# Kernel optimization log

Measured on AMD Instinct MI355X. Metric: run time of the kernel, lower is better.

The kernel has to match this reference:

```python
import jax, jax.numpy as jnp
import numpy as np

B, S, N = 16, 128, 64            # batch, sentence length, padded KB-word slots per sentence
E, DK, H, L = 128, 128, 128, 32  # char embed, kb embed, per-direction hidden (hidden_size=2H), labels
CHAR_NUM, KB_NUM = 8000, 200000


def setup_inputs():
    key = jax.random.key(0)
    ks = jax.random.split(key, 40)
    u = lambda k, sh: jax.random.uniform(k, sh, jnp.float32, -0.08, 0.08)
    inp = {
        "char_ids": jax.random.randint(ks[0], (B, S), 0, CHAR_NUM),
        "kb_word_ids": jax.random.randint(ks[1], (B, N), 0, KB_NUM),
        "word_begin": jax.random.randint(ks[2], (B, N), 0, S),
        "word_len": jax.random.randint(ks[3], (B, N), 0, 6),
        "label": jax.random.randint(ks[4], (B, S), 0, L),
        "sequence_length": jax.random.randint(ks[5], (B,), S // 2, S + 1),
        "char_emb": u(ks[6], (CHAR_NUM, E)),
        "kb_emb": u(ks[7], (KB_NUM, DK)),
        "dense_W": u(ks[8], (2 * H, L)),
        "dense_b": jnp.zeros((L,), jnp.float32),
        "crf_T": u(ks[9], (L, L)),
    }
    i = 10
    for p in ("f", "r"):
        inp[p + "_Wcx"] = u(ks[i], (E, 4 * H))
        inp[p + "_Wch"] = u(ks[i + 1], (H, 4 * H))
        inp[p + "_bc"] = jnp.zeros((4 * H,), jnp.float32)
        inp[p + "_Wwx"] = u(ks[i + 2], (DK, 3 * H))
        inp[p + "_Wwh"] = u(ks[i + 3], (H, 3 * H))
        inp[p + "_bw"] = jnp.zeros((3 * H,), jnp.float32)
        inp[p + "_Wlx"] = u(ks[i + 4], (E, H))
        inp[p + "_Wlc"] = u(ks[i + 5], (H, H))
        inp[p + "_bl"] = jnp.zeros((H,), jnp.float32)
        i += 6
    return inp


def _lattice_dir(X, Xw, begin, end, pos_valid, word_valid,
                 Wcx, Wch, bc, Wwx, Wwh, bw, Wlx, Wlc, bl):
    # X:[S,E] chars in scan order, Xw:[N,DK] KB words, begin/end:[N] span indices
    # in scan order (end inclusive), pos_valid:[S] bool, word_valid:[N] bool.
    Xg = X @ Wcx + bc    # [S,4H] hoisted char-gate input projection
    Xl = X @ Wlx + bl    # [S,H]  hoisted link-gate input projection
    Wg = Xw @ Wwx + bw   # [N,3H] hoisted word-gate input projection

    def step(carry, t):
        h_hist, c_hist = carry                 # [S+1,H]; slot k = state after step k-1
        h_prev, c_prev = h_hist[t], c_hist[t]
        gi, gf, go, gg = jnp.split(Xg[t] + h_prev @ Wch, 4)
        i = jax.nn.sigmoid(gi); f = jax.nn.sigmoid(gf)
        o = jax.nn.sigmoid(go); g = jnp.tanh(gg)
        # word cells: built from the state just before each word's begin position
        hb, cb = h_hist[begin], c_hist[begin]  # [N,H]
        wi, wf, wg = jnp.split(Wg + hb @ Wwh, 3, axis=1)
        cw = jax.nn.sigmoid(wf) * cb + jax.nn.sigmoid(wi) * jnp.tanh(wg)  # [N,H]
        lg = jax.nn.sigmoid(Xl[t] + cw @ Wlc)  # [N,H] link gates
        wmask = ((end == t) & word_valid).astype(X.dtype)[:, None]
        ew = jnp.exp(lg) * wmask
        ec = jnp.exp(i)
        c_lat = (ec * g + (ew * cw).sum(0)) / (ec + ew.sum(0))  # gate-normalized merge
        c_std = f * c_prev + i * g             # plain LSTM step when no word ends at t
        c_t = jnp.where(wmask.sum() > 0, c_lat, c_std)
        h_t = o * jnp.tanh(c_t)
        v = pos_valid[t]
        h_hist = h_hist.at[t + 1].set(jnp.where(v, h_t, h_prev))
        c_hist = c_hist.at[t + 1].set(jnp.where(v, c_t, c_prev))
        return (h_hist, c_hist), jnp.where(v, h_t, jnp.zeros_like(h_t))

    init = (jnp.zeros((S + 1, H), X.dtype), jnp.zeros((S + 1, H), X.dtype))
    _, hs = jax.lax.scan(step, init, jnp.arange(S))
    return hs  # [S,H]


def _forward(char_ids, kb_word_ids, word_begin, word_len, label, sequence_length,
             char_emb, kb_emb, dense_W, dense_b, crf_T, fparams, rparams):
    X = char_emb[char_ids]            # [B,S,E]
    Xw = kb_emb[kb_word_ids]          # [B,N,DK]
    end = jnp.minimum(word_begin + word_len, S - 1)   # inclusive span end
    word_valid = end < sequence_length[:, None]       # whole span inside sentence
    pos = jnp.arange(S)
    pv_f = pos[None, :] < sequence_length[:, None]
    fwd = jax.vmap(lambda x, xw, b, e, pv, wv:
                   _lattice_dir(x, xw, b, e, pv, wv, *fparams))(
        X, Xw, word_begin, end, pv_f, word_valid)
    # backward direction: flip time axis; span (b,e) maps to (S-1-e, S-1-b)
    pv_r = pos[None, :] >= (S - sequence_length)[:, None]
    bwd = jax.vmap(lambda x, xw, b, e, pv, wv:
                   _lattice_dir(x, xw, b, e, pv, wv, *rparams))(
        X[:, ::-1], Xw, S - 1 - end, S - 1 - word_begin, pv_r, word_valid)[:, ::-1]
    feats = jnp.concatenate([fwd, bwd], axis=-1)      # [B,S,2H]
    logits = feats @ dense_W + dense_b                # [B,S,L]
    # CRF negative log-likelihood
    mask = pv_f.astype(logits.dtype)                  # [B,S]
    emit = jnp.take_along_axis(logits, label[..., None], axis=2)[..., 0]
    trans = crf_T[label[:, :-1], label[:, 1:]]
    gold = (emit * mask).sum(1) + (trans * mask[:, 1:]).sum(1)

    def fstep(alpha, xs):
        logit_t, m_t = xs
        new = jax.scipy.special.logsumexp(alpha[:, :, None] + crf_T[None], axis=1) + logit_t
        return jnp.where(m_t[:, None] > 0, new, alpha), None

    alpha, _ = jax.lax.scan(fstep, logits[:, 0],
                            (logits[:, 1:].transpose(1, 0, 2), mask[:, 1:].T))
    logZ = jax.scipy.special.logsumexp(alpha, axis=1)
    return jnp.mean(logZ - gold)


def reference(char_ids, kb_word_ids, word_begin, word_len, label, sequence_length,
              char_emb, kb_emb, dense_W, dense_b, crf_T,
              f_Wcx, f_Wch, f_bc, f_Wwx, f_Wwh, f_bw, f_Wlx, f_Wlc, f_bl,
              r_Wcx, r_Wch, r_bc, r_Wwx, r_Wwh, r_bw, r_Wlx, r_Wlc, r_bl):
    fparams = (f_Wcx, f_Wch, f_bc, f_Wwx, f_Wwh, f_bw, f_Wlx, f_Wlc, f_bl)
    rparams = (r_Wcx, r_Wch, r_bc, r_Wwx, r_Wwh, r_bw, r_Wlx, r_Wlc, r_bl)
    return _forward(char_ids, kb_word_ids, word_begin, word_len, label, sequence_length,
                    char_emb, kb_emb, dense_W, dense_b, crf_T, fparams, rparams)
```

## Files before the change

kernel.cpp:

```cpp
#include <hip/hip_runtime.h>


typedef _Float16 f16x2 __attribute__((ext_vector_type(2)));

__device__ __forceinline__ float sigm(float x) { return 1.f / (1.f + __expf(-x)); }
__device__ __forceinline__ float tanh_fast(float x) {
    return 1.f - 2.f / (__expf(2.f * x) + 1.f);
}
__device__ __forceinline__ void bar_lgkm() {
    asm volatile("s_waitcnt lgkmcnt(0)\n\ts_barrier" ::: "memory");
}

#if defined(__has_builtin)
#if __has_builtin(__builtin_amdgcn_fdot2)
#define FDOT2(a, b, c) __builtin_amdgcn_fdot2((a), (b), (c), false)
#endif
#endif
#ifndef FDOT2
__device__ __forceinline__ float fdot2_sw(f16x2 a, f16x2 b, float c) {
    return fmaf((float)a.x, (float)b.x, fmaf((float)a.y, (float)b.y, c));
}
#define FDOT2(a, b, c) fdot2_sw((a), (b), (c))
#endif

template <int K, int J, int RPB, int BLK>
__global__ __launch_bounds__(BLK)
void gemm_pair(const float* __restrict__ emb, const int* __restrict__ idx,
               const float* __restrict__ W0, const float* __restrict__ W1,
               const float* __restrict__ b0, const float* __restrict__ b1,
               float* __restrict__ out, int rowsTotal, int Sdim, int revmode)
{
    constexpr int NJ4 = J / 4;
    constexpr int RT  = BLK / NJ4;
    constexpr int RPT = RPB / RT;
    static_assert(BLK % NJ4 == 0 && RPB % RT == 0, "layout");
    const int y = blockIdx.y;
    const float* __restrict__ W    = y ? W1 : W0;
    const float* __restrict__ bias = y ? b1 : b0;
    float* __restrict__ outp = out + (size_t)y * rowsTotal * J;
    const int rev = (revmode && y) ? 1 : 0;

    __shared__ __align__(16) float xs[RPB * K];
    __shared__ const float* srcs[RPB];
    const int tid = threadIdx.x;
    const int r0 = blockIdx.x * RPB;
    if (tid < RPB) {
        const int row = r0 + tid;
        const float* s = nullptr;
        if (row < rowsTotal) {
            if (idx) {
                const int bb = row / Sdim, tt = row - bb * Sdim;
                const int ts = rev ? (Sdim - 1 - tt) : tt;
                s = emb + (size_t)idx[bb * Sdim + ts] * K;
            } else {
                s = emb + (size_t)row * K;
            }
        }
        srcs[tid] = s;
    }
    __syncthreads();
    constexpr int NQ = RPB * K / 4;
    for (int q = tid; q < NQ; q += BLK) {
        const int rr = q / (K / 4), qq = q - rr * (K / 4);
        const float4* s = (const float4*)srcs[rr];
        ((float4*)xs)[q] = s ? s[qq] : make_float4(0.f, 0.f, 0.f, 0.f);
    }
    __syncthreads();

    const int jq = tid % NJ4;
    const int rg = tid / NJ4;
    float4 acc[RPT];
#pragma unroll
    for (int r = 0; r < RPT; ++r) acc[r] = make_float4(0.f, 0.f, 0.f, 0.f);
    const float4* __restrict__ W4 = (const float4*)W;
#pragma unroll 4
    for (int k = 0; k < K; ++k) {
        const float4 wv = W4[(size_t)k * NJ4 + jq];
#pragma unroll
        for (int r = 0; r < RPT; ++r) {
            const float xv = xs[(rg * RPT + r) * K + k];
            acc[r].x = fmaf(xv, wv.x, acc[r].x);
            acc[r].y = fmaf(xv, wv.y, acc[r].y);
            acc[r].z = fmaf(xv, wv.z, acc[r].z);
            acc[r].w = fmaf(xv, wv.w, acc[r].w);
        }
    }
    const float4 bv = ((const float4*)bias)[jq];
#pragma unroll
    for (int r = 0; r < RPT; ++r) {
        const int row = r0 + rg * RPT + r;
        if (row < rowsTotal)
            ((float4*)outp)[(size_t)row * NJ4 + jq] =
                make_float4(acc[r].x + bv.x, acc[r].y + bv.y,
                            acc[r].z + bv.z, acc[r].w + bv.w);
    }
}

#define HH_BYTES (129 * 128 * 2)
#define CH_BYTES (129 * 128 * 4)
#define LAT_DYN_SMEM (HH_BYTES + CH_BYTES)

__global__ __launch_bounds__(512, 2)
void lattice_kernel(const float* __restrict__ Xg,
                    const float* __restrict__ Xl,
                    const float* __restrict__ Wgp,
                    const float* __restrict__ Wch_f, const float* __restrict__ Wch_r,
                    const float* __restrict__ Wwh_f, const float* __restrict__ Wwh_r,
                    const float* __restrict__ Wlc_f, const float* __restrict__ Wlc_r,
                    const int* __restrict__ word_begin, const int* __restrict__ word_len,
                    const int* __restrict__ seqlen,
                    float* __restrict__ feats)
{
    extern __shared__ __align__(16) char dyn_smem[];
    _Float16* hh = (_Float16*)dyn_smem;
    float*    ch = (float*)(dyn_smem + HH_BYTES);

    const int bdid = blockIdx.x;
    const int b = bdid >> 1, dir = bdid & 1;
    const int tid = threadIdx.x;
    const int kc = tid >> 7;
    const int jj = tid & 127;

    const float* Wch = dir ? Wch_r : Wch_f;
    const float* Wwh = dir ? Wwh_r : Wwh_f;
    const float* Wlc = dir ? Wlc_r : Wlc_f;

    f16x2 wch2[64];
    {
        const float* base = Wch + (size_t)(kc * 32) * 512 + jj;
#pragma unroll
        for (int g = 0; g < 4; ++g)
#pragma unroll
            for (int u2 = 0; u2 < 16; ++u2) {
                f16x2 v;
                v.x = (_Float16)base[(size_t)(2 * u2) * 512 + g * 128];
                v.y = (_Float16)base[(size_t)(2 * u2 + 1) * 512 + g * 128];
                wch2[g * 16 + u2] = v;
            }
    }
    f16x2 wwh2[48];
    {
        const float* base = Wwh + (size_t)(kc * 32) * 384 + jj;
#pragma unroll
        for (int g = 0; g < 3; ++g)
#pragma unroll
            for (int u2 = 0; u2 < 16; ++u2) {
                f16x2 v;
                v.x = (_Float16)base[(size_t)(2 * u2) * 384 + g * 128];
                v.y = (_Float16)base[(size_t)(2 * u2 + 1) * 384 + g * 128];
                wwh2[g * 16 + u2] = v;
            }
    }
    f16x2 wlc2[16];
    {
        const float* base = Wlc + (size_t)(kc * 32) * 128 + jj;
#pragma unroll
        for (int u2 = 0; u2 < 16; ++u2) {
            f16x2 v;
            v.x = (_Float16)base[(size_t)(2 * u2) * 128];
            v.y = (_Float16)base[(size_t)(2 * u2 + 1) * 128];
            wlc2[u2] = v;
        }
    }

    __shared__ __align__(16) float part[2048];
    __shared__ __align__(16) float wpart[2 * 1536];
    __shared__ __align__(16) float lpart[2 * 512];
    __shared__ __align__(16) _Float16 cw2s[2 * 128];
    __shared__ int ev_start[129];
    __shared__ int cnts[128];
    __shared__ int fills[128];
    __shared__ short ev_word[64];
    __shared__ short wbeg_s[64];

    const int sl = seqlen[b];

    if (tid < 128) { cnts[tid] = 0; fills[tid] = 0; }
    __syncthreads();
    int myvalid = 0, myed = 0;
    if (tid < 64) {
        const int bg = word_begin[b * 64 + tid];
        const int ln = word_len[b * 64 + tid];
        int ef = bg + ln; if (ef > 127) ef = 127;
        myvalid = (ef < sl);
        const int bd_ = dir ? (127 - ef) : bg;
        const int ed_ = dir ? (127 - bg) : ef;
        wbeg_s[tid] = (short)bd_;
        myed = ed_;
        if (myvalid) atomicAdd(&cnts[ed_], 1);
    }
    __syncthreads();
    if (tid == 0) {
        int run = 0; ev_start[0] = 0;
        for (int t = 0; t < 128; ++t) { run += cnts[t]; ev_start[t + 1] = run; }
    }
    __syncthreads();
    if (tid < 64 && myvalid) {
        const int pos = atomicAdd(&fills[myed], 1);
        ev_word[ev_start[myed] + pos] = (short)tid;
    }
    if (tid < 128) { hh[tid] = (_Float16)0.f; ch[tid] = 0.f; }
    __syncthreads();

    const float* Xg_b = Xg + ((size_t)dir * 2048 + (size_t)b * 128) * 512;
    const float* Xl_b = Xl + ((size_t)dir * 2048 + (size_t)b * 128) * 128;
    const float* Wg_b = Wgp + ((size_t)dir * 1024 + (size_t)b * 64) * 384;

    float h_reg = 0.f, c_reg = 0.f;
    float xg_cur = Xg_b[tid];

    for (int t = 0; t < 128; ++t) {
        const int e0 = ev_start[t];
        const int E  = ev_start[t + 1] - e0;
        const int ec0 = E < 2 ? E : 2;

        int bgs[2] = {0, 0};
        float wgp[2][3];
        float xl = 0.f;
#pragma unroll
        for (int s = 0; s < 2; ++s)
            if (s < ec0) {
                const int w = ev_word[e0 + s];
                bgs[s] = wbeg_s[w];
                if (tid < 128) {
                    const float* wgr = Wg_b + (size_t)w * 384;
                    wgp[s][0] = wgr[tid]; wgp[s][1] = wgr[128 + tid]; wgp[s][2] = wgr[256 + tid];
                }
            }
        if (E > 0 && tid < 128) xl = Xl_b[(size_t)t * 128 + tid];
        const float xg_nxt = (t < 127) ? Xg_b[(size_t)(t + 1) * 512 + tid] : 0.f;

        {
            const f16x2* hrow = (const f16x2*)(hh + (size_t)t * 128) + kc * 16;
            f16x2 hv[16];
#pragma unroll
            for (int u2 = 0; u2 < 16; ++u2) hv[u2] = hrow[u2];
            float p0 = 0.f, p1 = 0.f, p2 = 0.f, p3 = 0.f;
#pragma unroll
            for (int u2 = 0; u2 < 16; ++u2) {
                p0 = FDOT2(wch2[u2],      hv[u2], p0);
                p1 = FDOT2(wch2[16 + u2], hv[u2], p1);
                p2 = FDOT2(wch2[32 + u2], hv[u2], p2);
                p3 = FDOT2(wch2[48 + u2], hv[u2], p3);
            }
            if      (kc == 0) p0 += xg_cur;
            else if (kc == 1) p1 += xg_cur;
            else if (kc == 2) p2 += xg_cur;
            else              p3 += xg_cur;
            part[kc * 512 +       jj] = p0;
            part[kc * 512 + 128 + jj] = p1;
            part[kc * 512 + 256 + jj] = p2;
            part[kc * 512 + 384 + jj] = p3;
        }
#pragma unroll
        for (int s = 0; s < 2; ++s)
            if (s < ec0) {
                const f16x2* hbrow = (const f16x2*)(hh + (size_t)bgs[s] * 128) + kc * 16;
                float q0 = 0.f, q1 = 0.f, q2 = 0.f;
#pragma unroll
                for (int u2 = 0; u2 < 16; ++u2) {
                    const f16x2 hb = hbrow[u2];
                    q0 = FDOT2(wwh2[u2],      hb, q0);
                    q1 = FDOT2(wwh2[16 + u2], hb, q1);
                    q2 = FDOT2(wwh2[32 + u2], hb, q2);
                }
                wpart[s * 1536 + kc * 384 +       jj] = q0;
                wpart[s * 1536 + kc * 384 + 128 + jj] = q1;
                wpart[s * 1536 + kc * 384 + 256 + jj] = q2;
            }
        bar_lgkm();

        float gi = 0.f, gf = 0.f, go = 0.f, gg = 0.f;
        float cwreg[2] = {0.f, 0.f};
        if (tid < 128) {
            const float a0 = part[tid]       + part[512 + tid]  + part[1024 + tid] + part[1536 + tid];
            const float a1 = part[128 + tid] + part[640 + tid]  + part[1152 + tid] + part[1664 + tid];
            const float a2 = part[256 + tid] + part[768 + tid]  + part[1280 + tid] + part[1792 + tid];
            const float a3 = part[384 + tid] + part[896 + tid]  + part[1408 + tid] + part[1920 + tid];
            gi = sigm(a0); gf = sigm(a1); go = sigm(a2); gg = tanh_fast(a3);
#pragma unroll
            for (int s = 0; s < 2; ++s)
                if (s < ec0) {
                    const int sb = s * 1536;
                    const float cb = ch[(size_t)bgs[s] * 128 + tid];
                    const float wi = wgp[s][0] + wpart[sb + tid]       + wpart[sb + 384 + tid] + wpart[sb + 768 + tid]  + wpart[sb + 1152 + tid];
                    const float wf = wgp[s][1] + wpart[sb + 128 + tid] + wpart[sb + 512 + tid] + wpart[sb + 896 + tid]  + wpart[sb + 1280 + tid];
                    const float wv = wgp[s][2] + wpart[sb + 256 + tid] + wpart[sb + 640 + tid] + wpart[sb + 1024 + tid] + wpart[sb + 1408 + tid];
                    const float cwv = sigm(wf) * cb + sigm(wi) * tanh_fast(wv);
                    cwreg[s] = cwv;
                    cw2s[s * 128 + tid] = (_Float16)cwv;
                }
        }

        float accn = 0.f, accd = 0.f;
        if (E > 0) {
            bar_lgkm();
            const int nc = (E + 1) >> 1;
            for (int c = 0; c < nc; ++c) {
                const int base = c * 2;
                const int en = (E - base) < 2 ? (E - base) : 2;
#pragma unroll
                for (int s = 0; s < 2; ++s)
                    if (s < en) {
                        const f16x2* cwrow = (const f16x2*)(cw2s + s * 128) + kc * 16;
                        float r = 0.f;
#pragma unroll
                        for (int u2 = 0; u2 < 16; ++u2) r = FDOT2(wlc2[u2], cwrow[u2], r);
                        lpart[s * 512 + kc * 128 + jj] = r;
                    }
                const int nb = base + 2;
                int nn = E - nb; nn = nn < 0 ? 0 : (nn > 2 ? 2 : nn);
                int bgs2[2] = {0, 0};
                float wgp2[2][3];
#pragma unroll
                for (int s = 0; s < 2; ++s)
                    if (s < nn) {
                        const int w = ev_word[e0 + nb + s];
                        bgs2[s] = wbeg_s[w];
                        if (tid < 128) {
                            const float* wgr = Wg_b + (size_t)w * 384;
                            wgp2[s][0] = wgr[tid]; wgp2[s][1] = wgr[128 + tid]; wgp2[s][2] = wgr[256 + tid];
                        }
                    }
#pragma unroll
                for (int s = 0; s < 2; ++s)
                    if (s < nn) {
                        const f16x2* hbrow = (const f16x2*)(hh + (size_t)bgs2[s] * 128) + kc * 16;
                        float q0 = 0.f, q1 = 0.f, q2 = 0.f;
#pragma unroll
                        for (int u2 = 0; u2 < 16; ++u2) {
                            const f16x2 hb = hbrow[u2];
                            q0 = FDOT2(wwh2[u2],      hb, q0);
                            q1 = FDOT2(wwh2[16 + u2], hb, q1);
                            q2 = FDOT2(wwh2[32 + u2], hb, q2);
                        }
                        wpart[s * 1536 + kc * 384 +       jj] = q0;
                        wpart[s * 1536 + kc * 384 + 128 + jj] = q1;
                        wpart[s * 1536 + kc * 384 + 256 + jj] = q2;
                    }
                bar_lgkm();
                if (tid < 128) {
#pragma unroll
                    for (int s = 0; s < 2; ++s)
                        if (s < en) {
                            const float lg = sigm(xl + lpart[s * 512 + tid] + lpart[s * 512 + 128 + tid]
                                                     + lpart[s * 512 + 256 + tid] + lpart[s * 512 + 384 + tid]);
                            const float ew = __expf(lg);
                            accn = fmaf(ew, cwreg[s], accn);
                            accd += ew;
                        }
#pragma unroll
                    for (int s = 0; s < 2; ++s)
                        if (s < nn) {
                            const int sb = s * 1536;
                            const float cb = ch[(size_t)bgs2[s] * 128 + tid];
                            const float wi = wgp2[s][0] + wpart[sb + tid]       + wpart[sb + 384 + tid] + wpart[sb + 768 + tid]  + wpart[sb + 1152 + tid];
                            const float wf = wgp2[s][1] + wpart[sb + 128 + tid] + wpart[sb + 512 + tid] + wpart[sb + 896 + tid]  + wpart[sb + 1280 + tid];
                            const float wv = wgp2[s][2] + wpart[sb + 256 + tid] + wpart[sb + 640 + tid] + wpart[sb + 1024 + tid] + wpart[sb + 1408 + tid];
                            const float cwv = sigm(wf) * cb + sigm(wi) * tanh_fast(wv);
                            cwreg[s] = cwv;
                            cw2s[s * 128 + tid] = (_Float16)cwv;
                        }
                }
                if (c + 1 < nc) bar_lgkm();
            }
        }

        if (tid < 128) {
            float c_t;
            if (E > 0) {
                const float ec = __expf(gi);
                c_t = (ec * gg + accn) / (ec + accd);
            } else {
                c_t = gf * c_reg + gi * gg;
            }
            const float h_t = go * tanh_fast(c_t);
            const bool v = dir ? (t >= 128 - sl) : (t < sl);
            const float hn = v ? h_t : h_reg;
            const float cn = v ? c_t : c_reg;
            h_reg = hn; c_reg = cn;
            hh[(size_t)(t + 1) * 128 + tid] = (_Float16)hn;
            ch[(size_t)(t + 1) * 128 + tid] = cn;
        }
        xg_cur = xg_nxt;
        bar_lgkm();
    }

    for (int i = tid; i < 128 * 128; i += 512) {
        const int t = i >> 7, j = i & 127;
        const bool v = dir ? (t >= 128 - sl) : (t < sl);
        const float hv = v ? (float)hh[(size_t)(t + 1) * 128 + j] : 0.f;
        const int s = dir ? (127 - t) : t;
        feats[((size_t)b * 128 + s) * 256 + dir * 128 + j] = hv;
    }
}

__global__ void crf_kernel(const float* __restrict__ logits,
                           const int* __restrict__ label,
                           const int* __restrict__ seqlen,
                           const float* __restrict__ T,
                           float* __restrict__ out_part)
{
    const int half = threadIdx.x >> 5;
    const int j    = threadIdx.x & 31;
    const int b    = blockIdx.x * 2 + half;

    float Tc[32];
#pragma unroll
    for (int i = 0; i < 32; ++i) Tc[i] = T[i * 32 + j];

    const float* lg = logits + (size_t)b * 128 * 32;
    const int* lab = label + b * 128;
    const int sl = seqlen[b];

    float g = 0.f;
#pragma unroll
    for (int r = 0; r < 4; ++r) {
        const int t = j + r * 32;
        if (t < sl) {
            g += lg[t * 32 + lab[t]];
            if (t >= 1) g += T[lab[t - 1] * 32 + lab[t]];
        }
    }
#pragma unroll
    for (int m = 16; m; m >>= 1) g += __shfl_xor(g, m, 32);

    __shared__ __align__(16) float alpha_s[2][32];
    float av = lg[j];
    alpha_s[half][j] = av;
    __syncthreads();
    for (int t = 1; t < 128; ++t) {
        float a[32];
        const float4* ap = (const float4*)alpha_s[half];
#pragma unroll
        for (int q = 0; q < 8; ++q) {
            const float4 v = ap[q];
            a[4 * q] = v.x; a[4 * q + 1] = v.y; a[4 * q + 2] = v.z; a[4 * q + 3] = v.w;
        }
        float m = -1e30f;
#pragma unroll
        for (int i = 0; i < 32; ++i) m = fmaxf(m, a[i] + Tc[i]);
        float s = 0.f;
#pragma unroll
        for (int i = 0; i < 32; ++i) s += __expf(a[i] + Tc[i] - m);
        float nv = m + __logf(s) + lg[t * 32 + j];
        if (t >= sl) nv = av;
        av = nv;
        __syncthreads();
        alpha_s[half][j] = av;
        __syncthreads();
    }
    float m2 = av;
#pragma unroll
    for (int m = 16; m; m >>= 1) m2 = fmaxf(m2, __shfl_xor(m2, m, 32));
    float s2 = __expf(av - m2);
#pragma unroll
    for (int m = 16; m; m >>= 1) s2 += __shfl_xor(s2, m, 32);
    if (j == 0) out_part[b] = (m2 + __logf(s2)) - g;
}

__global__ void finalize_kernel(const float* __restrict__ partb, float* __restrict__ out)
{
    if (threadIdx.x == 0 && blockIdx.x == 0) {
        float s = 0.f;
        for (int i = 0; i < 16; i++) s += partb[i];
        out[0] = s * (1.f / 16.f);
    }
}

extern "C" void kernel_launch(void* const* d_in, const int* in_sizes, int n_in,
                              void* d_out, int out_size, void* d_ws, size_t ws_size,
                              hipStream_t stream)
{
    (void)in_sizes; (void)n_in; (void)out_size; (void)ws_size;
    const int*   char_ids    = (const int*)d_in[0];
    const int*   kb_word_ids = (const int*)d_in[1];
    const int*   word_begin  = (const int*)d_in[2];
    const int*   word_len    = (const int*)d_in[3];
    const int*   label       = (const int*)d_in[4];
    const int*   seqlen      = (const int*)d_in[5];
    const float* char_emb    = (const float*)d_in[6];
    const float* kb_emb      = (const float*)d_in[7];
    const float* dense_W     = (const float*)d_in[8];
    const float* dense_b     = (const float*)d_in[9];
    const float* crf_T       = (const float*)d_in[10];
    const float* f_Wcx = (const float*)d_in[11];
    const float* f_Wch = (const float*)d_in[12];
    const float* f_bc  = (const float*)d_in[13];
    const float* f_Wwx = (const float*)d_in[14];
    const float* f_Wwh = (const float*)d_in[15];
    const float* f_bw  = (const float*)d_in[16];
    const float* f_Wlx = (const float*)d_in[17];
    const float* f_Wlc = (const float*)d_in[18];
    const float* f_bl  = (const float*)d_in[19];
    const float* r_Wcx = (const float*)d_in[20];
    const float* r_Wch = (const float*)d_in[21];
    const float* r_bc  = (const float*)d_in[22];
    const float* r_Wwx = (const float*)d_in[23];
    const float* r_Wwh = (const float*)d_in[24];
    const float* r_bw  = (const float*)d_in[25];
    const float* r_Wlx = (const float*)d_in[26];
    const float* r_Wlc = (const float*)d_in[27];
    const float* r_bl  = (const float*)d_in[28];

    float* ws = (float*)d_ws;
    size_t o = 0;
    float* Xg     = ws + o; o += (size_t)2 * 2048 * 512;
    float* Xl     = ws + o; o += (size_t)2 * 2048 * 128;
    float* Wg     = ws + o; o += (size_t)2 * 1024 * 384;
    float* feats  = ws + o; o += (size_t)2048 * 256;
    float* logits = ws + o; o += (size_t)2048 * 32;
    float* partb  = ws + o; o += 16;

    gemm_pair<128, 512, 8, 256><<<dim3(256, 2), 256, 0, stream>>>(
        char_emb, char_ids, f_Wcx, r_Wcx, f_bc, r_bc, Xg, 2048, 128, 1);
    gemm_pair<128, 128, 8, 256><<<dim3(256, 2), 256, 0, stream>>>(
        char_emb, char_ids, f_Wlx, r_Wlx, f_bl, r_bl, Xl, 2048, 128, 1);
    gemm_pair<128, 384, 8, 192><<<dim3(128, 2), 192, 0, stream>>>(
        kb_emb, kb_word_ids, f_Wwx, r_Wwx, f_bw, r_bw, Wg, 1024, 64, 0);

    lattice_kernel<<<32, 512, LAT_DYN_SMEM, stream>>>(
        Xg, Xl, Wg, f_Wch, r_Wch, f_Wwh, r_Wwh, f_Wlc, r_Wlc,
        word_begin, word_len, seqlen, feats);

    gemm_pair<256, 32, 16, 128><<<dim3(128, 1), 128, 0, stream>>>(
        feats, nullptr, dense_W, dense_W, dense_b, dense_b, logits, 2048, 128, 0);
    crf_kernel<<<8, 64, 0, stream>>>(logits, label, seqlen, crf_T, partb);
    finalize_kernel<<<1, 64, 0, stream>>>(partb, (float*)d_out);
}
```

Baseline: 540.6 us.

## Store hoisted projections in fp16 and stage them in LDS for the lattice scan

The input-projection GEMMs now write fp16 outputs, with Xg/Xl in a time-interleaved layout of 8-step blocks. The lattice kernel stages the per-sentence word projections in shared memory and double-buffers 8-step chunks of Xg/Xl in LDS, which takes global loads off the sequential critical path. The cell-state history is reduced to an 8-slot ring in LDS. The CRF kernel preloads logits and labels into shared memory, and the GEMM unroll and rows-per-block are raised. Risks are fp16 precision loss on the projections, and the c ring buffer breaks if a word span is longer than 8 steps (lengths here are at most 6).

```diff
diff --git a/kernel.cpp b/kernel.cpp
--- a/kernel.cpp
+++ b/kernel.cpp
@@ -23,12 +23,12 @@
 #define FDOT2(a, b, c) fdot2_sw((a), (b), (c))
 #endif
 
-template <int K, int J, int RPB, int BLK>
+template <int K, int J, int RPB, int BLK, int OMODE>
 __global__ __launch_bounds__(BLK)
 void gemm_pair(const float* __restrict__ emb, const int* __restrict__ idx,
                const float* __restrict__ W0, const float* __restrict__ W1,
                const float* __restrict__ b0, const float* __restrict__ b1,
-               float* __restrict__ out, int rowsTotal, int Sdim, int revmode)
+               void* __restrict__ out, int rowsTotal, int Sdim, int revmode)
 {
     constexpr int NJ4 = J / 4;
     constexpr int RT  = BLK / NJ4;
@@ -37,7 +37,6 @@
     const int y = blockIdx.y;
     const float* __restrict__ W    = y ? W1 : W0;
     const float* __restrict__ bias = y ? b1 : b0;
-    float* __restrict__ outp = out + (size_t)y * rowsTotal * J;
     const int rev = (revmode && y) ? 1 : 0;
 
     __shared__ __align__(16) float xs[RPB * K];
@@ -73,7 +72,7 @@
 #pragma unroll
     for (int r = 0; r < RPT; ++r) acc[r] = make_float4(0.f, 0.f, 0.f, 0.f);
     const float4* __restrict__ W4 = (const float4*)W;
-#pragma unroll 4
+#pragma unroll 8
     for (int k = 0; k < K; ++k) {
         const float4 wv = W4[(size_t)k * NJ4 + jq];
 #pragma unroll
@@ -89,21 +88,30 @@
 #pragma unroll
     for (int r = 0; r < RPT; ++r) {
         const int row = r0 + rg * RPT + r;
-        if (row < rowsTotal)
-            ((float4*)outp)[(size_t)row * NJ4 + jq] =
-                make_float4(acc[r].x + bv.x, acc[r].y + bv.y,
-                            acc[r].z + bv.z, acc[r].w + bv.w);
-    }
-}
-
-#define HH_BYTES (129 * 128 * 2)
-#define CH_BYTES (129 * 128 * 4)
-#define LAT_DYN_SMEM (HH_BYTES + CH_BYTES)
-
-__global__ __launch_bounds__(512, 2)
-void lattice_kernel(const float* __restrict__ Xg,
-                    const float* __restrict__ Xl,
-                    const float* __restrict__ Wgp,
+        if (row >= rowsTotal) continue;
+        float v4[4] = {acc[r].x + bv.x, acc[r].y + bv.y, acc[r].z + bv.z, acc[r].w + bv.w};
+        if constexpr (OMODE == 0) {
+            float* o32 = (float*)out + (size_t)y * rowsTotal * J;
+            ((float4*)o32)[(size_t)row * NJ4 + jq] = make_float4(v4[0], v4[1], v4[2], v4[3]);
+        } else if constexpr (OMODE == 1) {
+            _Float16* o16 = (_Float16*)out + (size_t)y * rowsTotal * J;
+            const size_t base = ((size_t)(row >> 3)) * (size_t)(J * 8) + (row & 7);
+#pragma unroll
+            for (int c = 0; c < 4; ++c)
+                o16[base + (size_t)(jq * 4 + c) * 8] = (_Float16)v4[c];
+        } else {
+            _Float16* o16 = (_Float16*)out + (size_t)y * rowsTotal * J;
+#pragma unroll
+            for (int c = 0; c < 4; ++c)
+                o16[(size_t)row * J + jq * 4 + c] = (_Float16)v4[c];
+        }
+    }
+}
+
+__global__ __launch_bounds__(512, 1)
+void lattice_kernel(const _Float16* __restrict__ Xg16,
+                    const _Float16* __restrict__ Xl16,
+                    const _Float16* __restrict__ Wg16G,
                     const float* __restrict__ Wch_f, const float* __restrict__ Wch_r,
                     const float* __restrict__ Wwh_f, const float* __restrict__ Wwh_r,
                     const float* __restrict__ Wlc_f, const float* __restrict__ Wlc_r,
@@ -111,10 +119,6 @@
                     const int* __restrict__ seqlen,
                     float* __restrict__ feats)
 {
-    extern __shared__ __align__(16) char dyn_smem[];
-    _Float16* hh = (_Float16*)dyn_smem;
-    float*    ch = (float*)(dyn_smem + HH_BYTES);
-
     const int bdid = blockIdx.x;
     const int b = bdid >> 1, dir = bdid & 1;
     const int tid = threadIdx.x;
@@ -125,6 +129,21 @@
     const float* Wwh = dir ? Wwh_r : Wwh_f;
     const float* Wlc = dir ? Wlc_r : Wlc_f;
 
+    __shared__ __align__(16) _Float16 wg16[64 * 384];
+    __shared__ __align__(16) _Float16 hh[129 * 128];
+    __shared__ __align__(16) float    c_win[8 * 128];
+    __shared__ __align__(16) float part[2048];
+    __shared__ __align__(16) float wpart[2 * 1536];
+    __shared__ __align__(16) float lpart[2 * 512];
+    __shared__ __align__(16) _Float16 cw2s[2 * 128];
+    __shared__ __align__(16) _Float16 xgbuf[2 * 4096];
+    __shared__ __align__(16) _Float16 xlbuf[2 * 1024];
+    __shared__ int ev_start[129];
+    __shared__ int cnts[128];
+    __shared__ int fills[128];
+    __shared__ short ev_word[64];
+    __shared__ short wbeg_s[64];
+
     f16x2 wch2[64];
     {
         const float* base = Wch + (size_t)(kc * 32) * 512 + jj;
@@ -162,16 +181,6 @@
             wlc2[u2] = v;
         }
     }
-
-    __shared__ __align__(16) float part[2048];
-    __shared__ __align__(16) float wpart[2 * 1536];
-    __shared__ __align__(16) float lpart[2 * 512];
-    __shared__ __align__(16) _Float16 cw2s[2 * 128];
-    __shared__ int ev_start[129];
-    __shared__ int cnts[128];
-    __shared__ int fills[128];
-    __shared__ short ev_word[64];
-    __shared__ short wbeg_s[64];
 
     const int sl = seqlen[b];
 
@@ -199,191 +208,205 @@
         const int pos = atomicAdd(&fills[myed], 1);
         ev_word[ev_start[myed] + pos] = (short)tid;
     }
-    if (tid < 128) { hh[tid] = (_Float16)0.f; ch[tid] = 0.f; }
-    __syncthreads();
-
-    const float* Xg_b = Xg + ((size_t)dir * 2048 + (size_t)b * 128) * 512;
-    const float* Xl_b = Xl + ((size_t)dir * 2048 + (size_t)b * 128) * 128;
-    const float* Wg_b = Wgp + ((size_t)dir * 1024 + (size_t)b * 64) * 384;
+    if (tid < 128) { hh[tid] = (_Float16)0.f; c_win[tid] = 0.f; }
+
+    {
+        const uint4* WgV = (const uint4*)(Wg16G + ((size_t)dir * 1024 + (size_t)b * 64) * 384);
+        uint4 wtmp[6];
+#pragma unroll
+        for (int i = 0; i < 6; ++i) wtmp[i] = WgV[i * 512 + tid];
+#pragma unroll
+        for (int i = 0; i < 6; ++i) ((uint4*)wg16)[i * 512 + tid] = wtmp[i];
+    }
+
+    const uint4* XgV = (const uint4*)(Xg16 + ((size_t)dir * 2048 + (size_t)b * 128) * 512);
+    const uint4* XlV = (const uint4*)(Xl16 + ((size_t)dir * 2048 + (size_t)b * 128) * 128);
+    uint4 xg_pre = XgV[tid];
+    uint4 xl_pre = make_uint4(0, 0, 0, 0);
+    if (tid < 128) xl_pre = XlV[tid];
+    __syncthreads();
 
     float h_reg = 0.f, c_reg = 0.f;
-    float xg_cur = Xg_b[tid];
-
-    for (int t = 0; t < 128; ++t) {
-        const int e0 = ev_start[t];
-        const int E  = ev_start[t + 1] - e0;
-        const int ec0 = E < 2 ? E : 2;
-
-        int bgs[2] = {0, 0};
-        float wgp[2][3];
-        float xl = 0.f;
-#pragma unroll
-        for (int s = 0; s < 2; ++s)
-            if (s < ec0) {
-                const int w = ev_word[e0 + s];
-                bgs[s] = wbeg_s[w];
-                if (tid < 128) {
-                    const float* wgr = Wg_b + (size_t)w * 384;
-                    wgp[s][0] = wgr[tid]; wgp[s][1] = wgr[128 + tid]; wgp[s][2] = wgr[256 + tid];
-                }
-            }
-        if (E > 0 && tid < 128) xl = Xl_b[(size_t)t * 128 + tid];
-        const float xg_nxt = (t < 127) ? Xg_b[(size_t)(t + 1) * 512 + tid] : 0.f;
-
-        {
-            const f16x2* hrow = (const f16x2*)(hh + (size_t)t * 128) + kc * 16;
-            f16x2 hv[16];
-#pragma unroll
-            for (int u2 = 0; u2 < 16; ++u2) hv[u2] = hrow[u2];
-            float p0 = 0.f, p1 = 0.f, p2 = 0.f, p3 = 0.f;
-#pragma unroll
-            for (int u2 = 0; u2 < 16; ++u2) {
-                p0 = FDOT2(wch2[u2],      hv[u2], p0);
-                p1 = FDOT2(wch2[16 + u2], hv[u2], p1);
-                p2 = FDOT2(wch2[32 + u2], hv[u2], p2);
-                p3 = FDOT2(wch2[48 + u2], hv[u2], p3);
-            }
-            if      (kc == 0) p0 += xg_cur;
-            else if (kc == 1) p1 += xg_cur;
-            else if (kc == 2) p2 += xg_cur;
-            else              p3 += xg_cur;
-            part[kc * 512 +       jj] = p0;
-            part[kc * 512 + 128 + jj] = p1;
-            part[kc * 512 + 256 + jj] = p2;
-            part[kc * 512 + 384 + jj] = p3;
-        }
-#pragma unroll
-        for (int s = 0; s < 2; ++s)
-            if (s < ec0) {
-                const f16x2* hbrow = (const f16x2*)(hh + (size_t)bgs[s] * 128) + kc * 16;
-                float q0 = 0.f, q1 = 0.f, q2 = 0.f;
-#pragma unroll
-                for (int u2 = 0; u2 < 16; ++u2) {
-                    const f16x2 hb = hbrow[u2];
-                    q0 = FDOT2(wwh2[u2],      hb, q0);
-                    q1 = FDOT2(wwh2[16 + u2], hb, q1);
-                    q2 = FDOT2(wwh2[32 + u2], hb, q2);
-                }
-                wpart[s * 1536 + kc * 384 +       jj] = q0;
-                wpart[s * 1536 + kc * 384 + 128 + jj] = q1;
-                wpart[s * 1536 + kc * 384 + 256 + jj] = q2;
-            }
+
+    for (int tc = 0; tc < 16; ++tc) {
+        _Float16* xgc = xgbuf + (tc & 1) * 4096;
+        _Float16* xlc = xlbuf + (tc & 1) * 1024;
+        ((uint4*)xgc)[tid] = xg_pre;
+        if (tid < 128) ((uint4*)xlc)[tid] = xl_pre;
+        if (tc < 15) {
+            xg_pre = XgV[(tc + 1) * 512 + tid];
+            if (tid < 128) xl_pre = XlV[(tc + 1) * 128 + tid];
+        }
         bar_lgkm();
 
-        float gi = 0.f, gf = 0.f, go = 0.f, gg = 0.f;
-        float cwreg[2] = {0.f, 0.f};
-        if (tid < 128) {
-            const float a0 = part[tid]       + part[512 + tid]  + part[1024 + tid] + part[1536 + tid];
-            const float a1 = part[128 + tid] + part[640 + tid]  + part[1152 + tid] + part[1664 + tid];
-            const float a2 = part[256 + tid] + part[768 + tid]  + part[1280 + tid] + part[1792 + tid];
-            const float a3 = part[384 + tid] + part[896 + tid]  + part[1408 + tid] + part[1920 + tid];
-            gi = sigm(a0); gf = sigm(a1); go = sigm(a2); gg = tanh_fast(a3);
+        for (int u = 0; u < 8; ++u) {
+            const int t = tc * 8 + u;
+            const int e0 = ev_start[t];
+            const int E  = ev_start[t + 1] - e0;
+            const int ec0 = E < 2 ? E : 2;
+
+            int bgs[2] = {0, 0}, wid[2] = {0, 0};
 #pragma unroll
             for (int s = 0; s < 2; ++s)
                 if (s < ec0) {
-                    const int sb = s * 1536;
-                    const float cb = ch[(size_t)bgs[s] * 128 + tid];
-                    const float wi = wgp[s][0] + wpart[sb + tid]       + wpart[sb + 384 + tid] + wpart[sb + 768 + tid]  + wpart[sb + 1152 + tid];
-                    const float wf = wgp[s][1] + wpart[sb + 128 + tid] + wpart[sb + 512 + tid] + wpart[sb + 896 + tid]  + wpart[sb + 1280 + tid];
-                    const float wv = wgp[s][2] + wpart[sb + 256 + tid] + wpart[sb + 640 + tid] + wpart[sb + 1024 + tid] + wpart[sb + 1408 + tid];
-                    const float cwv = sigm(wf) * cb + sigm(wi) * tanh_fast(wv);
-                    cwreg[s] = cwv;
-                    cw2s[s * 128 + tid] = (_Float16)cwv;
+                    const int w = ev_word[e0 + s];
+                    wid[s] = w; bgs[s] = wbeg_s[w];
                 }
-        }
-
-        float accn = 0.f, accd = 0.f;
-        if (E > 0) {
+            const float xg = (float)xgc[tid * 8 + u];
+
+            {
+                const f16x2* hrow = (const f16x2*)(hh + (size_t)t * 128) + kc * 16;
+                f16x2 hv[16];
+#pragma unroll
+                for (int u2 = 0; u2 < 16; ++u2) hv[u2] = hrow[u2];
+                float p0 = 0.f, p1 = 0.f, p2 = 0.f, p3 = 0.f;
+#pragma unroll
+                for (int u2 = 0; u2 < 16; ++u2) {
+                    p0 = FDOT2(wch2[u2],      hv[u2], p0);
+                    p1 = FDOT2(wch2[16 + u2], hv[u2], p1);
+                    p2 = FDOT2(wch2[32 + u2], hv[u2], p2);
+                    p3 = FDOT2(wch2[48 + u2], hv[u2], p3);
+                }
+                if      (kc == 0) p0 += xg;
+                else if (kc == 1) p1 += xg;
+                else if (kc == 2) p2 += xg;
+                else              p3 += xg;
+                part[kc * 512 +       jj] = p0;
+                part[kc * 512 + 128 + jj] = p1;
+                part[kc * 512 + 256 + jj] = p2;
+                part[kc * 512 + 384 + jj] = p3;
+            }
+#pragma unroll
+            for (int s = 0; s < 2; ++s)
+                if (s < ec0) {
+                    const f16x2* hbrow = (const f16x2*)(hh + (size_t)bgs[s] * 128) + kc * 16;
+                    float q0 = 0.f, q1 = 0.f, q2 = 0.f;
+#pragma unroll
+                    for (int u2 = 0; u2 < 16; ++u2) {
+                        const f16x2 hb = hbrow[u2];
+                        q0 = FDOT2(wwh2[u2],      hb, q0);
+                        q1 = FDOT2(wwh2[16 + u2], hb, q1);
+                        q2 = FDOT2(wwh2[32 + u2], hb, q2);
+                    }
+                    wpart[s * 1536 + kc * 384 +       jj] = q0;
+                    wpart[s * 1536 + kc * 384 + 128 + jj] = q1;
+                    wpart[s * 1536 + kc * 384 + 256 + jj] = q2;
+                }
             bar_lgkm();
-            const int nc = (E + 1) >> 1;
-            for (int c = 0; c < nc; ++c) {
-                const int base = c * 2;
-                const int en = (E - base) < 2 ? (E - base) : 2;
+
+            float gi = 0.f, gf = 0.f, go = 0.f, gg = 0.f;
+            float cwreg[2] = {0.f, 0.f};
+            if (tid < 128) {
+                const float a0 = part[tid]       + part[512 + tid]  + part[1024 + tid] + part[1536 + tid];
+                const float a1 = part[128 + tid] + part[640 + tid]  + part[1152 + tid] + part[1664 + tid];
+                const float a2 = part[256 + tid] + part[768 + tid]  + part[1280 + tid] + part[1792 + tid];
+                const float a3 = part[384 + tid] + part[896 + tid]  + part[1408 + tid] + part[1920 + tid];
+                gi = sigm(a0); gf = sigm(a1); go = sigm(a2); gg = tanh_fast(a3);
 #pragma unroll
                 for (int s = 0; s < 2; ++s)
-                    if (s < en) {
-                        const f16x2* cwrow = (const f16x2*)(cw2s + s * 128) + kc * 16;
-                        float r = 0.f;
-#pragma unroll
-                        for (int u2 = 0; u2 < 16; ++u2) r = FDOT2(wlc2[u2], cwrow[u2], r);
-                        lpart[s * 512 + kc * 128 + jj] = r;
+                    if (s < ec0) {
+                        const int sb = s * 1536;
+                        const _Float16* wgr = wg16 + wid[s] * 384;
+                        const float wi = (float)wgr[tid]       + wpart[sb + tid]       + wpart[sb + 384 + tid] + wpart[sb + 768 + tid]  + wpart[sb + 1152 + tid];
+                        const float wf = (float)wgr[128 + tid] + wpart[sb + 128 + tid] + wpart[sb + 512 + tid] + wpart[sb + 896 + tid]  + wpart[sb + 1280 + tid];
+                        const float wv = (float)wgr[256 + tid] + wpart[sb + 256 + tid] + wpart[sb + 640 + tid] + wpart[sb + 1024 + tid] + wpart[sb + 1408 + tid];
+                        const float cb = c_win[(bgs[s] & 7) * 128 + tid];
+                        const float cwv = sigm(wf) * cb + sigm(wi) * tanh_fast(wv);
+                        cwreg[s] = cwv;
+                        cw2s[s * 128 + tid] = (_Float16)cwv;
                     }
-                const int nb = base + 2;
-                int nn = E - nb; nn = nn < 0 ? 0 : (nn > 2 ? 2 : nn);
-                int bgs2[2] = {0, 0};
-                float wgp2[2][3];
-#pragma unroll
-                for (int s = 0; s < 2; ++s)
-                    if (s < nn) {
-                        const int w = ev_word[e0 + nb + s];
-                        bgs2[s] = wbeg_s[w];
-                        if (tid < 128) {
-                            const float* wgr = Wg_b + (size_t)w * 384;
-                            wgp2[s][0] = wgr[tid]; wgp2[s][1] = wgr[128 + tid]; wgp2[s][2] = wgr[256 + tid];
-                        }
-                    }
-#pragma unroll
-                for (int s = 0; s < 2; ++s)
-                    if (s < nn) {
-                        const f16x2* hbrow = (const f16x2*)(hh + (size_t)bgs2[s] * 128) + kc * 16;
-                        float q0 = 0.f, q1 = 0.f, q2 = 0.f;
-#pragma unroll
-                        for (int u2 = 0; u2 < 16; ++u2) {
-                            const f16x2 hb = hbrow[u2];
-                            q0 = FDOT2(wwh2[u2],      hb, q0);
-                            q1 = FDOT2(wwh2[16 + u2], hb, q1);
-                            q2 = FDOT2(wwh2[32 + u2], hb, q2);
-                        }
-                        wpart[s * 1536 + kc * 384 +       jj] = q0;
-                        wpart[s * 1536 + kc * 384 + 128 + jj] = q1;
-                        wpart[s * 1536 + kc * 384 + 256 + jj] = q2;
-                    }
+            }
+
+            float accn = 0.f, accd = 0.f;
+            if (E > 0) {
                 bar_lgkm();
-                if (tid < 128) {
+                const int nc = (E + 1) >> 1;
+                for (int c = 0; c < nc; ++c) {
+                    const int base = c * 2;
+                    const int en = (E - base) < 2 ? (E - base) : 2;
 #pragma unroll
                     for (int s = 0; s < 2; ++s)
                         if (s < en) {
-                            const float lg = sigm(xl + lpart[s * 512 + tid] + lpart[s * 512 + 128 + tid]
-                                                     + lpart[s * 512 + 256 + tid] + lpart[s * 512 + 384 + tid]);
-                            const float ew = __expf(lg);
-                            accn = fmaf(ew, cwreg[s], accn);
-                            accd += ew;
+                            const f16x2* cwrow = (const f16x2*)(cw2s + s * 128) + kc * 16;
+                            float r = 0.f;
+#pragma unroll
+                            for (int u2 = 0; u2 < 16; ++u2) r = FDOT2(wlc2[u2], cwrow[u2], r);
+                            lpart[s * 512 + kc * 128 + jj] = r;
                         }
+                    const int nb = base + 2;
+                    int nn = E - nb; nn = nn < 0 ? 0 : (nn > 2 ? 2 : nn);
+                    int bgs2[2] = {0, 0}, wid2[2] = {0, 0};
 #pragma unroll
                     for (int s = 0; s < 2; ++s)
                         if (s < nn) {
-                            const int sb = s * 1536;
-                            const float cb = ch[(size_t)bgs2[s] * 128 + tid];
-                            const float wi = wgp2[s][0] + wpart[sb + tid]       + wpart[sb + 384 + tid] + wpart[sb + 768 + tid]  + wpart[sb + 1152 + tid];
-                            const float wf = wgp2[s][1] + wpart[sb + 128 + tid] + wpart[sb + 512 + tid] + wpart[sb + 896 + tid]  + wpart[sb + 1280 + tid];
-                            const float wv = wgp2[s][2] + wpart[sb + 256 + tid] + wpart[sb + 640 + tid] + wpart[sb + 1024 + tid] + wpart[sb + 1408 + tid];
-                            const float cwv = sigm(wf) * cb + sigm(wi) * tanh_fast(wv);
-                            cwreg[s] = cwv;
-                            cw2s[s * 128 + tid] = (_Float16)cwv;
+                            const int w = ev_word[e0 + nb + s];
+                            wid2[s] = w; bgs2[s] = wbeg_s[w];
                         }
+#pragma unroll
+                    for (int s = 0; s < 2; ++s)
+                        if (s < nn) {
+                            const f16x2* hbrow = (const f16x2*)(hh + (size_t)bgs2[s] * 128) + kc * 16;
+                            float q0 = 0.f, q1 = 0.f, q2 = 0.f;
+#pragma unroll
+                            for (int u2 = 0; u2 < 16; ++u2) {
+                                const f16x2 hb = hbrow[u2];
+                                q0 = FDOT2(wwh2[u2],      hb, q0);
+                                q1 = FDOT2(wwh2[16 + u2], hb, q1);
+                                q2 = FDOT2(wwh2[32 + u2], hb, q2);
+                            }
+                            wpart[s * 1536 + kc * 384 +       jj] = q0;
+                            wpart[s * 1536 + kc * 384 + 128 + jj] = q1;
+                            wpart[s * 1536 + kc * 384 + 256 + jj] = q2;
+                        }
+                    bar_lgkm();
+                    if (tid < 128) {
+#pragma unroll
+                        for (int s = 0; s < 2; ++s)
+                            if (s < en) {
+                                const float lsum = (float)xlc[tid * 8 + u]
+                                    + lpart[s * 512 + tid] + lpart[s * 512 + 128 + tid]
+                                    + lpart[s * 512 + 256 + tid] + lpart[s * 512 + 384 + tid];
+                                const float lg = sigm(lsum);
+                                const float ew = __expf(lg);
+                                accn = fmaf(ew, cwreg[s], accn);
+                                accd += ew;
+                            }
+#pragma unroll
+                        for (int s = 0; s < 2; ++s)
+                            if (s < nn) {
+                                const int sb = s * 1536;
+                                const _Float16* wgr = wg16 + wid2[s] * 384;
+                                const float wi = (float)wgr[tid]       + wpart[sb + tid]       + wpart[sb + 384 + tid] + wpart[sb + 768 + tid]  + wpart[sb + 1152 + tid];
+                                const float wf = (float)wgr[128 + tid] + wpart[sb + 128 + tid] + wpart[sb + 512 + tid] + wpart[sb + 896 + tid]  + wpart[sb + 1280 + tid];
+                                const float wv = (float)wgr[256 + tid] + wpart[sb + 256 + tid] + wpart[sb + 640 + tid] + wpart[sb + 1024 + tid] + wpart[sb + 1408 + tid];
+                                const float cb = c_win[(bgs2[s] & 7) * 128 + tid];
+                                const float cwv = sigm(wf) * cb + sigm(wi) * tanh_fast(wv);
+                                cwreg[s] = cwv;
+                                cw2s[s * 128 + tid] = (_Float16)cwv;
+                            }
+                    }
+                    if (c + 1 < nc) bar_lgkm();
                 }
-                if (c + 1 < nc) bar_lgkm();
-            }
-        }
-
-        if (tid < 128) {
-            float c_t;
-            if (E > 0) {
-                const float ec = __expf(gi);
-                c_t = (ec * gg + accn) / (ec + accd);
-            } else {
-                c_t = gf * c_reg + gi * gg;
-            }
-            const float h_t = go * tanh_fast(c_t);
-            const bool v = dir ? (t >= 128 - sl) : (t < sl);
-            const float hn = v ? h_t : h_reg;
-            const float cn = v ? c_t : c_reg;
-            h_reg = hn; c_reg = cn;
-            hh[(size_t)(t + 1) * 128 + tid] = (_Float16)hn;
-            ch[(size_t)(t + 1) * 128 + tid] = cn;
-        }
-        xg_cur = xg_nxt;
-        bar_lgkm();
+            }
+
+            if (tid < 128) {
+                float c_t;
+                if (E > 0) {
+                    const float ec = __expf(gi);
+                    c_t = (ec * gg + accn) / (ec + accd);
+                } else {
+                    c_t = gf * c_reg + gi * gg;
+                }
+                const float h_t = go * tanh_fast(c_t);
+                const bool v = dir ? (t >= 128 - sl) : (t < sl);
+                const float hn = v ? h_t : h_reg;
+                const float cn = v ? c_t : c_reg;
+                h_reg = hn; c_reg = cn;
+                hh[(size_t)(t + 1) * 128 + tid] = (_Float16)hn;
+                c_win[((t + 1) & 7) * 128 + tid] = cn;
+            }
+            bar_lgkm();
+        }
     }
 
     for (int i = tid; i < 128 * 128; i += 512) {
@@ -395,38 +418,48 @@
     }
 }
 
-__global__ void crf_kernel(const float* __restrict__ logits,
-                           const int* __restrict__ label,
-                           const int* __restrict__ seqlen,
-                           const float* __restrict__ T,
-                           float* __restrict__ out_part)
+__global__ __launch_bounds__(64)
+void crf_kernel(const float* __restrict__ logits,
+                const int* __restrict__ label,
+                const int* __restrict__ seqlen,
+                const float* __restrict__ T,
+                float* __restrict__ out_part)
 {
     const int half = threadIdx.x >> 5;
     const int j    = threadIdx.x & 31;
     const int b    = blockIdx.x * 2 + half;
 
+    __shared__ __align__(16) float lgs[2][128 * 32];
+    __shared__ int labs[2][128];
+    __shared__ __align__(16) float alpha_s[2][32];
+
+    const float4* lg4 = (const float4*)(logits + (size_t)b * 4096);
+    float4* ls4 = (float4*)lgs[half];
+    for (int q = j; q < 1024; q += 32) ls4[q] = lg4[q];
+    for (int q = j; q < 128; q += 32) labs[half][q] = label[b * 128 + q];
+
     float Tc[32];
 #pragma unroll
     for (int i = 0; i < 32; ++i) Tc[i] = T[i * 32 + j];
-
-    const float* lg = logits + (size_t)b * 128 * 32;
-    const int* lab = label + b * 128;
+    __syncthreads();
+
     const int sl = seqlen[b];
+    const float* lgl = lgs[half];
+    const int* labl = labs[half];
 
     float g = 0.f;
 #pragma unroll
     for (int r = 0; r < 4; ++r) {
         const int t = j + r * 32;
         if (t < sl) {
-            g += lg[t * 32 + lab[t]];
-            if (t >= 1) g += T[lab[t - 1] * 32 + lab[t]];
+            g += lgl[t * 32 + labl[t]];
+            if (t >= 1) g += T[labl[t - 1] * 32 + labl[t]];
         }
     }
 #pragma unroll
     for (int m = 16; m; m >>= 1) g += __shfl_xor(g, m, 32);
 
-    __shared__ __align__(16) float alpha_s[2][32];
-    float av = lg[j];
+    float av = lgl[j];
     alpha_s[half][j] = av;
     __syncthreads();
     for (int t = 1; t < 128; ++t) {
@@ -443,7 +476,7 @@
         float s = 0.f;
 #pragma unroll
         for (int i = 0; i < 32; ++i) s += __expf(a[i] + Tc[i] - m);
-        float nv = m + __logf(s) + lg[t * 32 + j];
+        float nv = m + __logf(s) + lgl[t * 32 + j];
         if (t >= sl) nv = av;
         av = nv;
         __syncthreads();
@@ -503,27 +536,26 @@
     const float* r_Wlc = (const float*)d_in[27];
     const float* r_bl  = (const float*)d_in[28];
 
-    float* ws = (float*)d_ws;
-    size_t o = 0;
-    float* Xg     = ws + o; o += (size_t)2 * 2048 * 512;
-    float* Xl     = ws + o; o += (size_t)2 * 2048 * 128;
-    float* Wg     = ws + o; o += (size_t)2 * 1024 * 384;
-    float* feats  = ws + o; o += (size_t)2048 * 256;
-    float* logits = ws + o; o += (size_t)2048 * 32;
-    float* partb  = ws + o; o += 16;
-
-    gemm_pair<128, 512, 8, 256><<<dim3(256, 2), 256, 0, stream>>>(
-        char_emb, char_ids, f_Wcx, r_Wcx, f_bc, r_bc, Xg, 2048, 128, 1);
-    gemm_pair<128, 128, 8, 256><<<dim3(256, 2), 256, 0, stream>>>(
-        char_emb, char_ids, f_Wlx, r_Wlx, f_bl, r_bl, Xl, 2048, 128, 1);
-    gemm_pair<128, 384, 8, 192><<<dim3(128, 2), 192, 0, stream>>>(
-        kb_emb, kb_word_ids, f_Wwx, r_Wwx, f_bw, r_bw, Wg, 1024, 64, 0);
-
-    lattice_kernel<<<32, 512, LAT_DYN_SMEM, stream>>>(
-        Xg, Xl, Wg, f_Wch, r_Wch, f_Wwh, r_Wwh, f_Wlc, r_Wlc,
+    char* wsb = (char*)d_ws;
+    _Float16* Xg16 = (_Float16*)wsb; wsb += (size_t)2 * 2048 * 512 * 2;
+    _Float16* Xl16 = (_Float16*)wsb; wsb += (size_t)2 * 2048 * 128 * 2;
+    _Float16* Wg16 = (_Float16*)wsb; wsb += (size_t)2 * 1024 * 384 * 2;
+    float* feats   = (float*)wsb;    wsb += (size_t)2048 * 256 * 4;
+    float* logits  = (float*)wsb;    wsb += (size_t)2048 * 32 * 4;
+    float* partb   = (float*)wsb;
+
+    gemm_pair<128, 512, 16, 256, 1><<<dim3(128, 2), 256, 0, stream>>>(
+        char_emb, char_ids, f_Wcx, r_Wcx, f_bc, r_bc, Xg16, 2048, 128, 1);
+    gemm_pair<128, 128, 16, 256, 1><<<dim3(128, 2), 256, 0, stream>>>(
+        char_emb, char_ids, f_Wlx, r_Wlx, f_bl, r_bl, Xl16, 2048, 128, 1);
+    gemm_pair<128, 384, 16, 192, 2><<<dim3(64, 2), 192, 0, stream>>>(
+        kb_emb, kb_word_ids, f_Wwx, r_Wwx, f_bw, r_bw, Wg16, 1024, 64, 0);
+
+    lattice_kernel<<<32, 512, 0, stream>>>(
+        Xg16, Xl16, Wg16, f_Wch, r_Wch, f_Wwh, r_Wwh, f_Wlc, r_Wlc,
         word_begin, word_len, seqlen, feats);
 
-    gemm_pair<256, 32, 16, 128><<<dim3(128, 1), 128, 0, stream>>>(
+    gemm_pair<256, 32, 16, 128, 0><<<dim3(128, 1), 128, 0, stream>>>(
         feats, nullptr, dense_W, dense_W, dense_b, dense_b, logits, 2048, 128, 0);
     crf_kernel<<<8, 64, 0, stream>>>(logits, label, seqlen, crf_T, partb);
     finalize_kernel<<<1, 64, 0, stream>>>(partb, (float*)d_out);
```

Measured after the change: 596.5 us. +10.3%, slower.
